# Kernel tuning notes

Measured on AMD Instinct MI355X. Metric: run time of the kernel, lower is better.

Reference implementation:

```python
import jax, jax.numpy as jnp
import numpy as np

B, TOPK, MN = 128, 32, 64
MAX_NODES, H, E = 256, 128, 128
N_ENT, N_REL = 40000, 400


def setup_inputs() -> dict:
    key = jax.random.key(0)
    ks = jax.random.split(key, 11)
    s = 0.02  # weight init scale
    return {
        "node_embeddings": jax.random.normal(ks[0], (B, MAX_NODES + 2, H), jnp.float32),
        "entity_table": jax.random.normal(ks[1], (N_ENT, E), jnp.float32) * s,
        "relation_table": jax.random.normal(ks[2], (N_REL, E), jnp.float32) * s,
        "W_ih": jax.random.normal(ks[3], (3 * H, 2 * E), jnp.float32) * s,
        "W_hh": jax.random.normal(ks[4], (3 * H, H), jnp.float32) * s,
        "b_ih": jax.random.normal(ks[5], (3 * H,), jnp.float32) * s,
        "b_hh": jax.random.normal(ks[6], (3 * H,), jnp.float32) * s,
        "aim_nodes": jax.random.randint(ks[7], (B, TOPK), 0, MAX_NODES),
        "aim_entities": jax.random.randint(ks[8], (B, TOPK), 0, N_ENT),
        "neighbors": jax.random.randint(ks[9], (B, TOPK, MN, 2), 0, MAX_NODES + 2),
        "neighbors_num": jax.random.randint(ks[10], (B, TOPK), 0, MN + 1),
    }


def reference(node_embeddings, entity_table, relation_table, W_ih, W_hh, b_ih, b_hh,
              aim_nodes, aim_entities, neighbors, neighbors_num):
    # Agent.aggregate with use_rnn=True; returns updated node_embeddings.
    b, topk, mn, _ = neighbors.shape
    h_dim = node_embeddings.shape[-1]
    nb_nodes = neighbors[..., 0]      # (B, topk, mn) node positions
    nb_rel = neighbors[..., 1]        # (B, topk, mn) relation ids

    # per-batch gather of hidden states of neighbor nodes -> (B, topk, mn, H)
    h = jnp.take_along_axis(node_embeddings,
                            nb_nodes.reshape(b, topk * mn)[:, :, None],
                            axis=1).reshape(b, topk, mn, h_dim)
    ent = entity_table[aim_entities]          # (B, topk, E)
    rel = relation_table[nb_rel]              # (B, topk, mn, E)
    # GRU input: concat(aim entity embedding broadcast over neighbors, relation emb)
    x = jnp.concatenate(
        [jnp.broadcast_to(ent[:, :, None, :], rel.shape), rel], axis=-1)  # (B,topk,mn,2E)

    # torch GRUCell: gates ordered (r, z, n)
    gi = jnp.einsum('btme,ge->btmg', x, W_ih) + b_ih  # (B,topk,mn,3H)
    gh = jnp.einsum('btmh,gh->btmg', h, W_hh) + b_hh
    i_r, i_z, i_n = jnp.split(gi, 3, axis=-1)
    h_r, h_z, h_n = jnp.split(gh, 3, axis=-1)
    r = jax.nn.sigmoid(i_r + h_r)
    z = jax.nn.sigmoid(i_z + h_z)
    n = jnp.tanh(i_n + r * h_n)
    h_new = (1.0 - z) * n + z * h              # (B,topk,mn,H)

    # masked mean over valid neighbors (masked_fill(0) then sum / max(num,1))
    mask = jnp.arange(mn)[None, None, :] < neighbors_num[:, :, None]
    denom = neighbors_num.astype(h_new.dtype) + (neighbors_num == 0).astype(h_new.dtype)
    upd = jnp.where(mask[..., None], h_new, 0.0).sum(axis=2) / denom[..., None]  # (B,topk,H)

    # scatter updated representations back into the node table
    bidx = jnp.arange(b)[:, None]
    return node_embeddings.at[bidx, aim_nodes].set(upd)
```

## Files before the change

### kernel.cpp

```cpp
#include <hip/hip_runtime.h>

#define BB     128
#define TOPK   32
#define MN     64
#define NODES  258
#define NREL   400
#define SEG1_OFF 512
#define SEG2_OFF 4608
#define NROWS_TOT 37632
#define COLSPLIT 3

typedef __bf16 bf16x8 __attribute__((ext_vector_type(8)));
typedef float  f32x4  __attribute__((ext_vector_type(4)));

__device__ inline unsigned short f2bf(float f) {
    unsigned u = __float_as_uint(f);
    u = (u + 0x7fff + ((u >> 16) & 1)) >> 16;
    return (unsigned short)u;
}
__device__ inline float2 up2(unsigned u) {
    float2 r;
    r.x = __uint_as_float(u << 16);
    r.y = __uint_as_float(u & 0xffff0000u);
    return r;
}
__device__ inline float fsig(float x) {
    float e = __builtin_amdgcn_exp2f(-1.442695041f * x);
    return __builtin_amdgcn_rcpf(1.f + e);
}
__device__ inline float ftanh(float x) {
    x = fminf(15.f, fmaxf(-15.f, x));
    float e = __builtin_amdgcn_exp2f(2.885390082f * x);
    return (e - 1.f) * __builtin_amdgcn_rcpf(e + 1.f);
}

#define REGA_BLOCKS (NROWS_TOT * 16 / 256)
#define REGB_BLOCKS (147456 / 8 / 256)
__global__ __launch_bounds__(256) void prep(
        const float* __restrict__ node_emb, const float* __restrict__ ent_tab,
        const float* __restrict__ rel_tab, const int* __restrict__ aim_ent,
        const float* __restrict__ W_ih, const float* __restrict__ W_hh,
        const float* __restrict__ b_ih, const float* __restrict__ b_hh,
        unsigned short* __restrict__ A, unsigned short* __restrict__ Wpack,
        float* __restrict__ biasb, float* __restrict__ out) {
    int gid = blockIdx.x * 256 + threadIdx.x;
    if (blockIdx.x < REGA_BLOCKS) {
        int row = gid >> 4, kc = (gid & 15) << 3;
        float4 v0 = {0.f,0.f,0.f,0.f}, v1 = {0.f,0.f,0.f,0.f};
        if (row < NREL) {
            const float4* p = (const float4*)(rel_tab + (size_t)row * 128 + kc);
            v0 = p[0]; v1 = p[1];
        } else if (row < SEG1_OFF) {
        } else if (row < SEG2_OFF) {
            const float* e = ent_tab + (size_t)aim_ent[row - SEG1_OFF] * 128 + kc;
            v0 = ((const float4*)e)[0]; v1 = ((const float4*)e)[1];
        } else {
            int n = row - SEG2_OFF;
            const float4* p = (const float4*)(node_emb + (size_t)n * 128 + kc);
            v0 = p[0]; v1 = p[1];
            float4* o = (float4*)(out + (size_t)n * 128 + kc);
            o[0] = v0; o[1] = v1;
        }
        union { unsigned short s[8]; uint4 v; } u;
        u.s[0]=f2bf(v0.x); u.s[1]=f2bf(v0.y); u.s[2]=f2bf(v0.z); u.s[3]=f2bf(v0.w);
        u.s[4]=f2bf(v1.x); u.s[5]=f2bf(v1.y); u.s[6]=f2bf(v1.z); u.s[7]=f2bf(v1.w);
        *(uint4*)(A + (size_t)row * 128 + kc) = u.v;
    } else {
        int rb = gid - REGA_BLOCKS * 256;
        int e0 = rb * 8;
        int s = e0 / 49152, r = e0 % 49152;
        int n = r >> 7, k = r & 127;
        const float* src = (s == 0) ? (W_ih + n * 256 + 128 + k)
                         : (s == 1) ? (W_ih + n * 256 + k)
                                    : (W_hh + n * 128 + k);
        float4 v0 = ((const float4*)src)[0], v1 = ((const float4*)src)[1];
        union { unsigned short s[8]; uint4 v; } u;
        u.s[0]=f2bf(v0.x); u.s[1]=f2bf(v0.y); u.s[2]=f2bf(v0.z); u.s[3]=f2bf(v0.w);
        u.s[4]=f2bf(v1.x); u.s[5]=f2bf(v1.y); u.s[6]=f2bf(v1.z); u.s[7]=f2bf(v1.w);
        *(uint4*)(Wpack + e0) = u.v;
        if (rb < 144) {
            for (int j = 0; j < 8; ++j) {
                int e = rb * 8 + j;
                int s2 = e / 384, g = e % 384;
                biasb[e] = (s2 == 0) ? 0.f : (s2 == 1 ? b_ih[g] : b_hh[g]);
            }
        }
    }
}

__global__ __launch_bounds__(256) void mfma_gemm(
        const unsigned short* __restrict__ A, const unsigned short* __restrict__ Wpack,
        const float* __restrict__ biasb, unsigned short* __restrict__ G) {
    __shared__ __align__(16) unsigned short Bs[128 * 128];
    const int tid = threadIdx.x;
    const int w = tid >> 6, lane = tid & 63;
    const int rb = blockIdx.x / COLSPLIT, cs = blockIdx.x % COLSPLIT;
    const int brow = rb * 128;
    const int row0 = brow + w * 32;
    const int seg  = (brow < SEG1_OFF) ? 0 : (brow < SEG2_OFF ? 1 : 2);
    const int limit = (seg == 0) ? NREL : NROWS_TOT;
    const int colbase = cs * 128;
    const unsigned short* Wt = Wpack + (size_t)seg * 49152 + (size_t)colbase * 128;

#pragma unroll
    for (int ii = 0; ii < 8; ++ii) {
        int dst = ii * 256 + tid;
        int g = dst >> 6, rem = dst & 63;
        int qq = rem >> 4, cc = rem & 15;
        int tt = g >> 2, kbb = g & 3;
        uint4 v = *(const uint4*)(Wt + (size_t)(tt * 16 + cc) * 128 + kbb * 32 + qq * 8);
        *(uint4*)(Bs + dst * 8) = v;
    }

    const int q = lane >> 4, c = lane & 15;
    const int koff = q << 3;
    bf16x8 a0[4], a1[4];
    {
        const unsigned short* Ar0 = A + (size_t)(row0 + c) * 128 + koff;
        const unsigned short* Ar1 = Ar0 + 16 * 128;
#pragma unroll
        for (int kb = 0; kb < 4; ++kb) {
            a0[kb] = *(const bf16x8*)(Ar0 + kb * 32);
            a1[kb] = *(const bf16x8*)(Ar1 + kb * 32);
        }
    }
    float bv[8];
#pragma unroll
    for (int t = 0; t < 8; ++t)
        bv[t] = biasb[seg * 384 + colbase + t * 16 + c];

    __syncthreads();

    const int r0 = row0 + q * 4, r1 = r0 + 16;
#pragma unroll 2
    for (int t = 0; t < 8; ++t) {
        bf16x8 bf[4];
#pragma unroll
        for (int kb = 0; kb < 4; ++kb)
            bf[kb] = *(const bf16x8*)(Bs + (size_t)((t * 4 + kb) * 64 + lane) * 8);
        f32x4 acc0 = {0.f,0.f,0.f,0.f}, acc1 = {0.f,0.f,0.f,0.f};
#pragma unroll
        for (int kb = 0; kb < 4; ++kb) {
            acc0 = __builtin_amdgcn_mfma_f32_16x16x32_bf16(a0[kb], bf[kb], acc0, 0, 0, 0);
            acc1 = __builtin_amdgcn_mfma_f32_16x16x32_bf16(a1[kb], bf[kb], acc1, 0, 0, 0);
        }
        const int gc = colbase + t * 16 + c;
#pragma unroll
        for (int i2 = 0; i2 < 4; ++i2) {
            if (r0 + i2 < limit) G[(size_t)(r0 + i2) * 384 + gc] = f2bf(acc0[i2] + bv[t]);
            if (r1 + i2 < limit) G[(size_t)(r1 + i2) * 384 + gc] = f2bf(acc1[i2] + bv[t]);
        }
    }
}

__global__ __launch_bounds__(512) void gru_agg(
        const unsigned short* __restrict__ A, const unsigned short* __restrict__ G,
        const int* __restrict__ aim_nodes, const int* __restrict__ neighbors,
        const int* __restrict__ nb_num, float* __restrict__ out) {
    const int bt = blockIdx.x;
    const int b = bt >> 5, t = bt & 31;
    const int tid = threadIdx.x;
    const int w = tid >> 6, lane = tid & 63;

    const int myaim = aim_nodes[bt];
    for (int t2 = t + 1; t2 < TOPK; ++t2)
        if (aim_nodes[b * TOPK + t2] == myaim) return;

    __shared__ int2 nbs[MN];
    __shared__ float2 part[8][64];
    if (tid < MN) nbs[tid] = ((const int2*)neighbors)[(size_t)bt * MN + tid];
    __syncthreads();

    int num = nb_num[bt];
    num = (num < 0) ? 0 : (num > MN ? MN : num);

    const unsigned short* Gl = G + 2 * lane;
    const unsigned short* Ge = Gl + (size_t)(SEG1_OFF + bt) * 384;
    const float2 ge_r = up2(*(const unsigned*)(Ge));
    const float2 ge_z = up2(*(const unsigned*)(Ge + 128));
    const float2 ge_n = up2(*(const unsigned*)(Ge + 256));

    const unsigned short* Gh = Gl + ((size_t)SEG2_OFF + (size_t)b * NODES) * 384;
    const unsigned short* Av = A + ((size_t)SEG2_OFF + (size_t)b * NODES) * 128 + 2 * lane;

    float2 acc = {0.f, 0.f};
    for (int m = w; m < num; m += 8) {
        int2 p = nbs[m];
        const unsigned short* gr = Gl + (size_t)p.y * 384;
        const unsigned short* gh = Gh + (size_t)p.x * 384;
        unsigned ur0 = *(const unsigned*)(gr);
        unsigned ur1 = *(const unsigned*)(gr + 128);
        unsigned ur2 = *(const unsigned*)(gr + 256);
        unsigned uh0 = *(const unsigned*)(gh);
        unsigned uh1 = *(const unsigned*)(gh + 128);
        unsigned uh2 = *(const unsigned*)(gh + 256);
        unsigned uv  = *(const unsigned*)(Av + (size_t)p.x * 128);
        float2 r0 = up2(ur0), r1 = up2(ur1), r2 = up2(ur2);
        float2 h0 = up2(uh0), h1 = up2(uh1), h2 = up2(uh2);
        float2 hv = up2(uv);
        float rx = fsig(ge_r.x + r0.x + h0.x);
        float zx = fsig(ge_z.x + r1.x + h1.x);
        float nx = ftanh(ge_n.x + r2.x + rx * h2.x);
        acc.x += (1.f - zx) * nx + zx * hv.x;
        float ry = fsig(ge_r.y + r0.y + h0.y);
        float zy = fsig(ge_z.y + r1.y + h1.y);
        float ny = ftanh(ge_n.y + r2.y + ry * h2.y);
        acc.y += (1.f - zy) * ny + zy * hv.y;
    }
    part[w][lane] = acc;
    __syncthreads();
    if (tid < 64) {
        float2 s = part[0][lane];
#pragma unroll
        for (int k = 1; k < 8; ++k) { s.x += part[k][lane].x; s.y += part[k][lane].y; }
        const float denom = (num > 0) ? (float)num : 1.f;
        const float sc = __builtin_amdgcn_rcpf(denom);
        float2 r; r.x = s.x * sc; r.y = s.y * sc;
        *(float2*)(out + ((size_t)b * NODES + myaim) * 128 + 2 * lane) = r;
    }
}

extern "C" void kernel_launch(void* const* d_in, const int* in_sizes, int n_in,
                              void* d_out, int out_size, void* d_ws, size_t ws_size,
                              hipStream_t stream) {
    const float* node_emb = (const float*)d_in[0];
    const float* ent_tab  = (const float*)d_in[1];
    const float* rel_tab  = (const float*)d_in[2];
    const float* W_ih     = (const float*)d_in[3];
    const float* W_hh     = (const float*)d_in[4];
    const float* b_ih     = (const float*)d_in[5];
    const float* b_hh     = (const float*)d_in[6];
    const int* aim_nodes  = (const int*)d_in[7];
    const int* aim_ent    = (const int*)d_in[8];
    const int* neighbors  = (const int*)d_in[9];
    const int* nb_num     = (const int*)d_in[10];
    float* out = (float*)d_out;

    unsigned short* G     = (unsigned short*)d_ws;
    unsigned short* A     = G + (size_t)NROWS_TOT * 384;
    unsigned short* Wpack = A + (size_t)NROWS_TOT * 128;
    float*          biasb = (float*)(Wpack + 3 * 384 * 128);

    hipLaunchKernelGGL(prep, dim3(REGA_BLOCKS + REGB_BLOCKS), dim3(256), 0, stream,
                       node_emb, ent_tab, rel_tab, aim_ent, W_ih, W_hh, b_ih, b_hh,
                       A, Wpack, biasb, out);
    hipLaunchKernelGGL(mfma_gemm, dim3((NROWS_TOT / 128) * COLSPLIT), dim3(256), 0, stream,
                       A, Wpack, biasb, G);
    hipLaunchKernelGGL(gru_agg, dim3(BB * TOPK), dim3(512), 0, stream,
                       A, G, aim_nodes, neighbors, nb_num, out);
}
```

Baseline: 146.4 us.

## Fuse bf16 conversion prep into GEMM kernel and drop intermediate A buffer

Removes the separate prep kernel. The GEMM now loads fp32 activations and weights directly and converts them to bf16 in registers before the MFMA. The node-embedding copy to the output runs as extra blocks in the same launch, and the GRU kernel reads fp32 h straight from node_emb instead of the bf16 A copy. This cuts one launch and the write/read of the intermediate A, Wpack and bias buffers, at the cost of every GEMM block redundantly converting its weight tile.

New measurement: 152.2 us. 1.04x slower.

```diff
diff --git a/kernel.cpp b/kernel.cpp
--- a/kernel.cpp
+++ b/kernel.cpp
@@ -9,6 +9,8 @@
 #define SEG2_OFF 4608
 #define NROWS_TOT 37632
 #define COLSPLIT 3
+#define GEMM_BLOCKS ((NROWS_TOT / 128) * COLSPLIT)
+#define COPY_BLOCKS 2064
 
 typedef __bf16 bf16x8 __attribute__((ext_vector_type(8)));
 typedef float  f32x4  __attribute__((ext_vector_type(4)));
@@ -17,6 +19,17 @@
     unsigned u = __float_as_uint(f);
     u = (u + 0x7fff + ((u >> 16) & 1)) >> 16;
     return (unsigned short)u;
+}
+__device__ inline uint4 conv8(float4 a, float4 b) {
+    union { unsigned short s[8]; uint4 v; } u;
+    u.s[0]=f2bf(a.x); u.s[1]=f2bf(a.y); u.s[2]=f2bf(a.z); u.s[3]=f2bf(a.w);
+    u.s[4]=f2bf(b.x); u.s[5]=f2bf(b.y); u.s[6]=f2bf(b.z); u.s[7]=f2bf(b.w);
+    return u.v;
+}
+__device__ inline bf16x8 conv8f(float4 a, float4 b) {
+    union { uint4 v; bf16x8 b8; } u;
+    u.v = conv8(a, b);
+    return u.b8;
 }
 __device__ inline float2 up2(unsigned u) {
     float2 r;
@@ -34,65 +47,24 @@
     return (e - 1.f) * __builtin_amdgcn_rcpf(e + 1.f);
 }
 
-#define REGA_BLOCKS (NROWS_TOT * 16 / 256)
-#define REGB_BLOCKS (147456 / 8 / 256)
-__global__ __launch_bounds__(256) void prep(
+__global__ __launch_bounds__(256) void gemm_mega(
         const float* __restrict__ node_emb, const float* __restrict__ ent_tab,
-        const float* __restrict__ rel_tab, const int* __restrict__ aim_ent,
-        const float* __restrict__ W_ih, const float* __restrict__ W_hh,
-        const float* __restrict__ b_ih, const float* __restrict__ b_hh,
-        unsigned short* __restrict__ A, unsigned short* __restrict__ Wpack,
-        float* __restrict__ biasb, float* __restrict__ out) {
-    int gid = blockIdx.x * 256 + threadIdx.x;
-    if (blockIdx.x < REGA_BLOCKS) {
-        int row = gid >> 4, kc = (gid & 15) << 3;
-        float4 v0 = {0.f,0.f,0.f,0.f}, v1 = {0.f,0.f,0.f,0.f};
-        if (row < NREL) {
-            const float4* p = (const float4*)(rel_tab + (size_t)row * 128 + kc);
-            v0 = p[0]; v1 = p[1];
-        } else if (row < SEG1_OFF) {
-        } else if (row < SEG2_OFF) {
-            const float* e = ent_tab + (size_t)aim_ent[row - SEG1_OFF] * 128 + kc;
-            v0 = ((const float4*)e)[0]; v1 = ((const float4*)e)[1];
-        } else {
-            int n = row - SEG2_OFF;
-            const float4* p = (const float4*)(node_emb + (size_t)n * 128 + kc);
-            v0 = p[0]; v1 = p[1];
-            float4* o = (float4*)(out + (size_t)n * 128 + kc);
-            o[0] = v0; o[1] = v1;
-        }
-        union { unsigned short s[8]; uint4 v; } u;
-        u.s[0]=f2bf(v0.x); u.s[1]=f2bf(v0.y); u.s[2]=f2bf(v0.z); u.s[3]=f2bf(v0.w);
-        u.s[4]=f2bf(v1.x); u.s[5]=f2bf(v1.y); u.s[6]=f2bf(v1.z); u.s[7]=f2bf(v1.w);
-        *(uint4*)(A + (size_t)row * 128 + kc) = u.v;
-    } else {
-        int rb = gid - REGA_BLOCKS * 256;
-        int e0 = rb * 8;
-        int s = e0 / 49152, r = e0 % 49152;
-        int n = r >> 7, k = r & 127;
-        const float* src = (s == 0) ? (W_ih + n * 256 + 128 + k)
-                         : (s == 1) ? (W_ih + n * 256 + k)
-                                    : (W_hh + n * 128 + k);
-        float4 v0 = ((const float4*)src)[0], v1 = ((const float4*)src)[1];
-        union { unsigned short s[8]; uint4 v; } u;
-        u.s[0]=f2bf(v0.x); u.s[1]=f2bf(v0.y); u.s[2]=f2bf(v0.z); u.s[3]=f2bf(v0.w);
-        u.s[4]=f2bf(v1.x); u.s[5]=f2bf(v1.y); u.s[6]=f2bf(v1.z); u.s[7]=f2bf(v1.w);
-        *(uint4*)(Wpack + e0) = u.v;
-        if (rb < 144) {
-            for (int j = 0; j < 8; ++j) {
-                int e = rb * 8 + j;
-                int s2 = e / 384, g = e % 384;
-                biasb[e] = (s2 == 0) ? 0.f : (s2 == 1 ? b_ih[g] : b_hh[g]);
-            }
-        }
-    }
-}
-
-__global__ __launch_bounds__(256) void mfma_gemm(
-        const unsigned short* __restrict__ A, const unsigned short* __restrict__ Wpack,
-        const float* __restrict__ biasb, unsigned short* __restrict__ G) {
+        const float* __restrict__ rel_tab, const float* __restrict__ W_ih,
+        const float* __restrict__ W_hh, const float* __restrict__ b_ih,
+        const float* __restrict__ b_hh, const int* __restrict__ aim_ent,
+        unsigned short* __restrict__ G, float* __restrict__ out) {
     __shared__ __align__(16) unsigned short Bs[128 * 128];
     const int tid = threadIdx.x;
+
+    if (blockIdx.x >= GEMM_BLOCKS) {
+        size_t base = ((size_t)(blockIdx.x - GEMM_BLOCKS) * 256 + tid) * 8;
+        float4 v0 = *(const float4*)(node_emb + base);
+        float4 v1 = *(const float4*)(node_emb + base + 4);
+        *(float4*)(out + base)     = v0;
+        *(float4*)(out + base + 4) = v1;
+        return;
+    }
+
     const int w = tid >> 6, lane = tid & 63;
     const int rb = blockIdx.x / COLSPLIT, cs = blockIdx.x % COLSPLIT;
     const int brow = rb * 128;
@@ -100,7 +72,6 @@
     const int seg  = (brow < SEG1_OFF) ? 0 : (brow < SEG2_OFF ? 1 : 2);
     const int limit = (seg == 0) ? NREL : NROWS_TOT;
     const int colbase = cs * 128;
-    const unsigned short* Wt = Wpack + (size_t)seg * 49152 + (size_t)colbase * 128;
 
 #pragma unroll
     for (int ii = 0; ii < 8; ++ii) {
@@ -108,26 +79,52 @@
         int g = dst >> 6, rem = dst & 63;
         int qq = rem >> 4, cc = rem & 15;
         int tt = g >> 2, kbb = g & 3;
-        uint4 v = *(const uint4*)(Wt + (size_t)(tt * 16 + cc) * 128 + kbb * 32 + qq * 8);
-        *(uint4*)(Bs + dst * 8) = v;
+        int n = colbase + tt * 16 + cc, k = kbb * 32 + qq * 8;
+        const float* src = (seg == 0) ? (W_ih + n * 256 + 128 + k)
+                         : (seg == 1) ? (W_ih + n * 256 + k)
+                                      : (W_hh + n * 128 + k);
+        float4 w0 = ((const float4*)src)[0], w1 = ((const float4*)src)[1];
+        *(uint4*)(Bs + dst * 8) = conv8(w0, w1);
     }
 
     const int q = lane >> 4, c = lane & 15;
     const int koff = q << 3;
+    const int arow = row0 + c;
     bf16x8 a0[4], a1[4];
     {
-        const unsigned short* Ar0 = A + (size_t)(row0 + c) * 128 + koff;
-        const unsigned short* Ar1 = Ar0 + 16 * 128;
+        const float *s0, *s1;
+        bool v0 = true, v1 = true;
+        if (seg == 0) {
+            v0 = arow < NREL; v1 = (arow + 16) < NREL;
+            s0 = rel_tab + (size_t)(v0 ? arow : 0) * 128;
+            s1 = rel_tab + (size_t)(v1 ? (arow + 16) : 0) * 128;
+        } else if (seg == 1) {
+            s0 = ent_tab + (size_t)aim_ent[arow - SEG1_OFF] * 128;
+            s1 = ent_tab + (size_t)aim_ent[arow - SEG1_OFF + 16] * 128;
+        } else {
+            s0 = node_emb + (size_t)(arow - SEG2_OFF) * 128;
+            s1 = s0 + 16 * 128;
+        }
+        const float4 z4 = {0.f, 0.f, 0.f, 0.f};
 #pragma unroll
         for (int kb = 0; kb < 4; ++kb) {
-            a0[kb] = *(const bf16x8*)(Ar0 + kb * 32);
-            a1[kb] = *(const bf16x8*)(Ar1 + kb * 32);
+            int k = kb * 32 + koff;
+            float4 x0 = ((const float4*)(s0 + k))[0];
+            float4 x1 = ((const float4*)(s0 + k))[1];
+            float4 y0 = ((const float4*)(s1 + k))[0];
+            float4 y1 = ((const float4*)(s1 + k))[1];
+            if (!v0) { x0 = z4; x1 = z4; }
+            if (!v1) { y0 = z4; y1 = z4; }
+            a0[kb] = conv8f(x0, x1);
+            a1[kb] = conv8f(y0, y1);
         }
     }
     float bv[8];
 #pragma unroll
-    for (int t = 0; t < 8; ++t)
-        bv[t] = biasb[seg * 384 + colbase + t * 16 + c];
+    for (int t = 0; t < 8; ++t) {
+        int gc = colbase + t * 16 + c;
+        bv[t] = (seg == 0) ? 0.f : (seg == 1 ? b_ih[gc] : b_hh[gc]);
+    }
 
     __syncthreads();
 
@@ -154,7 +151,7 @@
 }
 
 __global__ __launch_bounds__(512) void gru_agg(
-        const unsigned short* __restrict__ A, const unsigned short* __restrict__ G,
+        const float* __restrict__ node_emb, const unsigned short* __restrict__ G,
         const int* __restrict__ aim_nodes, const int* __restrict__ neighbors,
         const int* __restrict__ nb_num, float* __restrict__ out) {
     const int bt = blockIdx.x;
@@ -166,10 +163,7 @@
     for (int t2 = t + 1; t2 < TOPK; ++t2)
         if (aim_nodes[b * TOPK + t2] == myaim) return;
 
-    __shared__ int2 nbs[MN];
     __shared__ float2 part[8][64];
-    if (tid < MN) nbs[tid] = ((const int2*)neighbors)[(size_t)bt * MN + tid];
-    __syncthreads();
 
     int num = nb_num[bt];
     num = (num < 0) ? 0 : (num > MN ? MN : num);
@@ -181,11 +175,12 @@
     const float2 ge_n = up2(*(const unsigned*)(Ge + 256));
 
     const unsigned short* Gh = Gl + ((size_t)SEG2_OFF + (size_t)b * NODES) * 384;
-    const unsigned short* Av = A + ((size_t)SEG2_OFF + (size_t)b * NODES) * 128 + 2 * lane;
+    const float* hb = node_emb + (size_t)b * NODES * 128 + 2 * lane;
+    const int2* nbp = (const int2*)neighbors + (size_t)bt * MN;
 
     float2 acc = {0.f, 0.f};
     for (int m = w; m < num; m += 8) {
-        int2 p = nbs[m];
+        int2 p = nbp[m];
         const unsigned short* gr = Gl + (size_t)p.y * 384;
         const unsigned short* gh = Gh + (size_t)p.x * 384;
         unsigned ur0 = *(const unsigned*)(gr);
@@ -194,10 +189,9 @@
         unsigned uh0 = *(const unsigned*)(gh);
         unsigned uh1 = *(const unsigned*)(gh + 128);
         unsigned uh2 = *(const unsigned*)(gh + 256);
-        unsigned uv  = *(const unsigned*)(Av + (size_t)p.x * 128);
+        float2 hv = *(const float2*)(hb + (size_t)p.x * 128);
         float2 r0 = up2(ur0), r1 = up2(ur1), r2 = up2(ur2);
         float2 h0 = up2(uh0), h1 = up2(uh1), h2 = up2(uh2);
-        float2 hv = up2(uv);
         float rx = fsig(ge_r.x + r0.x + h0.x);
         float zx = fsig(ge_z.x + r1.x + h1.x);
         float nx = ftanh(ge_n.x + r2.x + rx * h2.x);
@@ -236,16 +230,11 @@
     const int* nb_num     = (const int*)d_in[10];
     float* out = (float*)d_out;
 
-    unsigned short* G     = (unsigned short*)d_ws;
-    unsigned short* A     = G + (size_t)NROWS_TOT * 384;
-    unsigned short* Wpack = A + (size_t)NROWS_TOT * 128;
-    float*          biasb = (float*)(Wpack + 3 * 384 * 128);
-
-    hipLaunchKernelGGL(prep, dim3(REGA_BLOCKS + REGB_BLOCKS), dim3(256), 0, stream,
-                       node_emb, ent_tab, rel_tab, aim_ent, W_ih, W_hh, b_ih, b_hh,
-                       A, Wpack, biasb, out);
-    hipLaunchKernelGGL(mfma_gemm, dim3((NROWS_TOT / 128) * COLSPLIT), dim3(256), 0, stream,
-                       A, Wpack, biasb, G);
+    unsigned short* G = (unsigned short*)d_ws;
+
+    hipLaunchKernelGGL(gemm_mega, dim3(GEMM_BLOCKS + COPY_BLOCKS), dim3(256), 0, stream,
+                       node_emb, ent_tab, rel_tab, W_ih, W_hh, b_ih, b_hh, aim_ent,
+                       G, out);
     hipLaunchKernelGGL(gru_agg, dim3(BB * TOPK), dim3(512), 0, stream,
-                       A, G, aim_nodes, neighbors, nb_num, out);
-}
+                       node_emb, G, aim_nodes, neighbors, nb_num, out);
+}
```

## Fuse weight bf16 packing into GEMM, remap GRU blocks per XCD, drop LDS neighbor staging

Applied to the files above, without the earlier changes.

Removes the separate weight/bias packing from the prep kernel, so each GEMM block now reads fp32 W_ih/W_hh and biases directly and converts them to bf16 while filling shared memory. The gru_agg block index is remapped so blocks landing on the same XCD handle the same batch, aiming to improve L2 reuse of that batch's node rows in G and A. Neighbor pairs are read straight from global memory instead of being staged in LDS behind a barrier. In exchange, every GEMM block reconverts the weights, which means more redundant fp32 reads and conversion work.

Measured after the change: 147.1 us. Within noise of the previous version (+0.5%).

```diff
diff --git a/kernel.cpp b/kernel.cpp
--- a/kernel.cpp
+++ b/kernel.cpp
@@ -9,6 +9,7 @@
 #define SEG2_OFF 4608
 #define NROWS_TOT 37632
 #define COLSPLIT 3
+#define GEMM_BLOCKS ((NROWS_TOT / 128) * COLSPLIT)
 
 typedef __bf16 bf16x8 __attribute__((ext_vector_type(8)));
 typedef float  f32x4  __attribute__((ext_vector_type(4)));
@@ -17,6 +18,12 @@
     unsigned u = __float_as_uint(f);
     u = (u + 0x7fff + ((u >> 16) & 1)) >> 16;
     return (unsigned short)u;
+}
+__device__ inline uint4 conv8(float4 a, float4 b) {
+    union { unsigned short s[8]; uint4 v; } u;
+    u.s[0]=f2bf(a.x); u.s[1]=f2bf(a.y); u.s[2]=f2bf(a.z); u.s[3]=f2bf(a.w);
+    u.s[4]=f2bf(b.x); u.s[5]=f2bf(b.y); u.s[6]=f2bf(b.z); u.s[7]=f2bf(b.w);
+    return u.v;
 }
 __device__ inline float2 up2(unsigned u) {
     float2 r;
@@ -34,63 +41,34 @@
     return (e - 1.f) * __builtin_amdgcn_rcpf(e + 1.f);
 }
 
-#define REGA_BLOCKS (NROWS_TOT * 16 / 256)
-#define REGB_BLOCKS (147456 / 8 / 256)
 __global__ __launch_bounds__(256) void prep(
         const float* __restrict__ node_emb, const float* __restrict__ ent_tab,
         const float* __restrict__ rel_tab, const int* __restrict__ aim_ent,
-        const float* __restrict__ W_ih, const float* __restrict__ W_hh,
-        const float* __restrict__ b_ih, const float* __restrict__ b_hh,
-        unsigned short* __restrict__ A, unsigned short* __restrict__ Wpack,
-        float* __restrict__ biasb, float* __restrict__ out) {
+        unsigned short* __restrict__ A, float* __restrict__ out) {
     int gid = blockIdx.x * 256 + threadIdx.x;
-    if (blockIdx.x < REGA_BLOCKS) {
-        int row = gid >> 4, kc = (gid & 15) << 3;
-        float4 v0 = {0.f,0.f,0.f,0.f}, v1 = {0.f,0.f,0.f,0.f};
-        if (row < NREL) {
-            const float4* p = (const float4*)(rel_tab + (size_t)row * 128 + kc);
-            v0 = p[0]; v1 = p[1];
-        } else if (row < SEG1_OFF) {
-        } else if (row < SEG2_OFF) {
-            const float* e = ent_tab + (size_t)aim_ent[row - SEG1_OFF] * 128 + kc;
-            v0 = ((const float4*)e)[0]; v1 = ((const float4*)e)[1];
-        } else {
-            int n = row - SEG2_OFF;
-            const float4* p = (const float4*)(node_emb + (size_t)n * 128 + kc);
-            v0 = p[0]; v1 = p[1];
-            float4* o = (float4*)(out + (size_t)n * 128 + kc);
-            o[0] = v0; o[1] = v1;
-        }
-        union { unsigned short s[8]; uint4 v; } u;
-        u.s[0]=f2bf(v0.x); u.s[1]=f2bf(v0.y); u.s[2]=f2bf(v0.z); u.s[3]=f2bf(v0.w);
-        u.s[4]=f2bf(v1.x); u.s[5]=f2bf(v1.y); u.s[6]=f2bf(v1.z); u.s[7]=f2bf(v1.w);
-        *(uint4*)(A + (size_t)row * 128 + kc) = u.v;
+    int row = gid >> 4, kc = (gid & 15) << 3;
+    float4 v0 = {0.f,0.f,0.f,0.f}, v1 = {0.f,0.f,0.f,0.f};
+    if (row < NREL) {
+        const float4* p = (const float4*)(rel_tab + (size_t)row * 128 + kc);
+        v0 = p[0]; v1 = p[1];
+    } else if (row < SEG1_OFF) {
+    } else if (row < SEG2_OFF) {
+        const float* e = ent_tab + (size_t)aim_ent[row - SEG1_OFF] * 128 + kc;
+        v0 = ((const float4*)e)[0]; v1 = ((const float4*)e)[1];
     } else {
-        int rb = gid - REGA_BLOCKS * 256;
-        int e0 = rb * 8;
-        int s = e0 / 49152, r = e0 % 49152;
-        int n = r >> 7, k = r & 127;
-        const float* src = (s == 0) ? (W_ih + n * 256 + 128 + k)
-                         : (s == 1) ? (W_ih + n * 256 + k)
-                                    : (W_hh + n * 128 + k);
-        float4 v0 = ((const float4*)src)[0], v1 = ((const float4*)src)[1];
-        union { unsigned short s[8]; uint4 v; } u;
-        u.s[0]=f2bf(v0.x); u.s[1]=f2bf(v0.y); u.s[2]=f2bf(v0.z); u.s[3]=f2bf(v0.w);
-        u.s[4]=f2bf(v1.x); u.s[5]=f2bf(v1.y); u.s[6]=f2bf(v1.z); u.s[7]=f2bf(v1.w);
-        *(uint4*)(Wpack + e0) = u.v;
-        if (rb < 144) {
-            for (int j = 0; j < 8; ++j) {
-                int e = rb * 8 + j;
-                int s2 = e / 384, g = e % 384;
-                biasb[e] = (s2 == 0) ? 0.f : (s2 == 1 ? b_ih[g] : b_hh[g]);
-            }
-        }
-    }
+        int n = row - SEG2_OFF;
+        const float4* p = (const float4*)(node_emb + (size_t)n * 128 + kc);
+        v0 = p[0]; v1 = p[1];
+        float4* o = (float4*)(out + (size_t)n * 128 + kc);
+        o[0] = v0; o[1] = v1;
+    }
+    *(uint4*)(A + (size_t)row * 128 + kc) = conv8(v0, v1);
 }
 
 __global__ __launch_bounds__(256) void mfma_gemm(
-        const unsigned short* __restrict__ A, const unsigned short* __restrict__ Wpack,
-        const float* __restrict__ biasb, unsigned short* __restrict__ G) {
+        const unsigned short* __restrict__ A, const float* __restrict__ W_ih,
+        const float* __restrict__ W_hh, const float* __restrict__ b_ih,
+        const float* __restrict__ b_hh, unsigned short* __restrict__ G) {
     __shared__ __align__(16) unsigned short Bs[128 * 128];
     const int tid = threadIdx.x;
     const int w = tid >> 6, lane = tid & 63;
@@ -100,7 +78,6 @@
     const int seg  = (brow < SEG1_OFF) ? 0 : (brow < SEG2_OFF ? 1 : 2);
     const int limit = (seg == 0) ? NREL : NROWS_TOT;
     const int colbase = cs * 128;
-    const unsigned short* Wt = Wpack + (size_t)seg * 49152 + (size_t)colbase * 128;
 
 #pragma unroll
     for (int ii = 0; ii < 8; ++ii) {
@@ -108,8 +85,12 @@
         int g = dst >> 6, rem = dst & 63;
         int qq = rem >> 4, cc = rem & 15;
         int tt = g >> 2, kbb = g & 3;
-        uint4 v = *(const uint4*)(Wt + (size_t)(tt * 16 + cc) * 128 + kbb * 32 + qq * 8);
-        *(uint4*)(Bs + dst * 8) = v;
+        int n = colbase + tt * 16 + cc, k = kbb * 32 + qq * 8;
+        const float* src = (seg == 0) ? (W_ih + n * 256 + 128 + k)
+                         : (seg == 1) ? (W_ih + n * 256 + k)
+                                      : (W_hh + n * 128 + k);
+        float4 w0 = ((const float4*)src)[0], w1 = ((const float4*)src)[1];
+        *(uint4*)(Bs + dst * 8) = conv8(w0, w1);
     }
 
     const int q = lane >> 4, c = lane & 15;
@@ -126,8 +107,10 @@
     }
     float bv[8];
 #pragma unroll
-    for (int t = 0; t < 8; ++t)
-        bv[t] = biasb[seg * 384 + colbase + t * 16 + c];
+    for (int t = 0; t < 8; ++t) {
+        int gc = colbase + t * 16 + c;
+        bv[t] = (seg == 0) ? 0.f : (seg == 1 ? b_ih[gc] : b_hh[gc]);
+    }
 
     __syncthreads();
 
@@ -157,8 +140,11 @@
         const unsigned short* __restrict__ A, const unsigned short* __restrict__ G,
         const int* __restrict__ aim_nodes, const int* __restrict__ neighbors,
         const int* __restrict__ nb_num, float* __restrict__ out) {
-    const int bt = blockIdx.x;
-    const int b = bt >> 5, t = bt & 31;
+    const int idx = blockIdx.x;
+    const int xcd = idx & 7, slot = idx >> 3;
+    const int b = (slot >> 5) * 8 + xcd;
+    const int t = slot & 31;
+    const int bt = b * TOPK + t;
     const int tid = threadIdx.x;
     const int w = tid >> 6, lane = tid & 63;
 
@@ -166,10 +152,7 @@
     for (int t2 = t + 1; t2 < TOPK; ++t2)
         if (aim_nodes[b * TOPK + t2] == myaim) return;
 
-    __shared__ int2 nbs[MN];
     __shared__ float2 part[8][64];
-    if (tid < MN) nbs[tid] = ((const int2*)neighbors)[(size_t)bt * MN + tid];
-    __syncthreads();
 
     int num = nb_num[bt];
     num = (num < 0) ? 0 : (num > MN ? MN : num);
@@ -182,10 +165,11 @@
 
     const unsigned short* Gh = Gl + ((size_t)SEG2_OFF + (size_t)b * NODES) * 384;
     const unsigned short* Av = A + ((size_t)SEG2_OFF + (size_t)b * NODES) * 128 + 2 * lane;
+    const int2* nbp = (const int2*)neighbors + (size_t)bt * MN;
 
     float2 acc = {0.f, 0.f};
     for (int m = w; m < num; m += 8) {
-        int2 p = nbs[m];
+        int2 p = nbp[m];
         const unsigned short* gr = Gl + (size_t)p.y * 384;
         const unsigned short* gh = Gh + (size_t)p.x * 384;
         unsigned ur0 = *(const unsigned*)(gr);
@@ -236,16 +220,13 @@
     const int* nb_num     = (const int*)d_in[10];
     float* out = (float*)d_out;
 
-    unsigned short* G     = (unsigned short*)d_ws;
-    unsigned short* A     = G + (size_t)NROWS_TOT * 384;
-    unsigned short* Wpack = A + (size_t)NROWS_TOT * 128;
-    float*          biasb = (float*)(Wpack + 3 * 384 * 128);
-
-    hipLaunchKernelGGL(prep, dim3(REGA_BLOCKS + REGB_BLOCKS), dim3(256), 0, stream,
-                       node_emb, ent_tab, rel_tab, aim_ent, W_ih, W_hh, b_ih, b_hh,
-                       A, Wpack, biasb, out);
-    hipLaunchKernelGGL(mfma_gemm, dim3((NROWS_TOT / 128) * COLSPLIT), dim3(256), 0, stream,
-                       A, Wpack, biasb, G);
+    unsigned short* G = (unsigned short*)d_ws;
+    unsigned short* A = G + (size_t)NROWS_TOT * 384;
+
+    hipLaunchKernelGGL(prep, dim3(NROWS_TOT * 16 / 256), dim3(256), 0, stream,
+                       node_emb, ent_tab, rel_tab, aim_ent, A, out);
+    hipLaunchKernelGGL(mfma_gemm, dim3(GEMM_BLOCKS), dim3(256), 0, stream,
+                       A, W_ih, W_hh, b_ih, b_hh, G);
     hipLaunchKernelGGL(gru_agg, dim3(BB * TOPK), dim3(512), 0, stream,
                        A, G, aim_nodes, neighbors, nb_num, out);
 }
```
